# Kernel optimization log

Measured on AMD Instinct MI355X. Metric: run time of the kernel, lower is better.

The kernel has to match this reference:

```python
import jax, jax.numpy as jnp
import numpy as np

EPS = 1e-5

def _bn(x, g, b):
    # training-mode BatchNorm1d over the batch axis (axis 0), biased variance
    m = jnp.mean(x, axis=0)
    v = jnp.var(x, axis=0)
    return g * (x - m) / jnp.sqrt(v + EPS) + b

def _mlp(x, w1, b1, g1, be1, w2, b2, g2, be2, w3, b3):
    # Linear -> BN -> ReLU -> Linear -> BN -> ReLU -> Linear
    x = jax.nn.relu(_bn(x @ w1.T + b1, g1, be1))
    x = jax.nn.relu(_bn(x @ w2.T + b2, g2, be2))
    return x @ w3.T + b3

def setup_inputs() -> dict:
    key = jax.random.key(0)
    ks = jax.random.split(key, 10)
    B, S, D = 256, 512, 128
    w = lambda k: jax.random.normal(k, (D, D), jnp.float32) * 0.05
    return {
        "s": jax.random.normal(ks[0], (B, S, D), jnp.float32),
        "c": jax.random.normal(ks[1], (B, D), jnp.float32),
        "s_w1": w(ks[2]), "s_b1": jnp.zeros((D,), jnp.float32),
        "s_g1": jnp.ones((D,), jnp.float32), "s_be1": jnp.zeros((D,), jnp.float32),
        "s_w2": w(ks[3]), "s_b2": jnp.zeros((D,), jnp.float32),
        "s_g2": jnp.ones((D,), jnp.float32), "s_be2": jnp.zeros((D,), jnp.float32),
        "s_w3": w(ks[4]), "s_b3": jnp.zeros((D,), jnp.float32),
        "c_w1": w(ks[5]), "c_b1": jnp.zeros((D,), jnp.float32),
        "c_g1": jnp.ones((D,), jnp.float32), "c_be1": jnp.zeros((D,), jnp.float32),
        "c_w2": w(ks[6]), "c_b2": jnp.zeros((D,), jnp.float32),
        "c_g2": jnp.ones((D,), jnp.float32), "c_be2": jnp.zeros((D,), jnp.float32),
        "c_w3": w(ks[7]), "c_b3": jnp.zeros((D,), jnp.float32),
    }

def reference(s, c,
              s_w1, s_b1, s_g1, s_be1, s_w2, s_b2, s_g2, s_be2, s_w3, s_b3,
              c_w1, c_b1, c_g1, c_be1, c_w2, c_b2, c_g2, c_be2, c_w3, c_b3):
    # c_mlp: [B, D] -> [B, D] (BN over batch)
    c_out = _mlp(c, c_w1, c_b1, c_g1, c_be1, c_w2, c_b2, c_g2, c_be2, c_w3, c_b3)
    # s_mlp applied per sequence slice; BN stats over batch axis 0 only
    # (matches the torch loop where each s[:, i, :] gets its own BN stats).
    # s: [B, S, D]; _bn with axis=0 gives per-(slice, feature) stats.
    s_h = _mlp(s, s_w1, s_b1, s_g1, s_be1, s_w2, s_b2, s_g2, s_be2, s_w3, s_b3)
    s_out = s_h * c_out[:, None, :]          # context gate, [B, S, D]
    aggregated_c = jnp.max(s_out, axis=1)    # pooling == 'max', [B, D]
    return (s_out, aggregated_c)
```

## Files before the change

### kernel.cpp

```cpp
#include <hip/hip_runtime.h>
#include <hip/hip_bf16.h>

#define BATCH 256
#define SEQ   512
#define DIM   128
#define LDSK  136

typedef __attribute__((ext_vector_type(8))) __bf16  bf16x8;
typedef __attribute__((ext_vector_type(4))) __bf16  bf16x4;
typedef __attribute__((ext_vector_type(4))) float   f32x4;

template<int RT>
__device__ __forceinline__ void matmul_layer(
    const __bf16* __restrict__ Xa, const __bf16* __restrict__ wg,
    const float* __restrict__ bias, f32x4 (&acc)[RT][8], int wave, int m, int q)
{
  const int rowbase = wave * RT * 16;
#pragma unroll
  for (int ct = 0; ct < 8; ++ct) {
    const float b = bias[ct * 16 + m];
    const f32x4 bv = {b, b, b, b};
#pragma unroll
    for (int rt = 0; rt < RT; ++rt) acc[rt][ct] = bv;
  }
#pragma unroll
  for (int ks = 0; ks < 4; ++ks) {
    const int k0 = ks * 32 + q * 8;
    bf16x8 a[RT], bw[8];
#pragma unroll
    for (int rt = 0; rt < RT; ++rt)
      a[rt] = *(const bf16x8*)(Xa + (rowbase + rt * 16 + m) * LDSK + k0);
#pragma unroll
    for (int ct = 0; ct < 8; ++ct)
      bw[ct] = *(const bf16x8*)(wg + (ct * 16 + m) * DIM + k0);
#pragma unroll
    for (int rt = 0; rt < RT; ++rt)
#pragma unroll
      for (int ct = 0; ct < 8; ++ct)
        acc[rt][ct] = __builtin_amdgcn_mfma_f32_16x16x32_bf16(a[rt], bw[ct], acc[rt][ct], 0, 0, 0);
  }
}

template<int RT>
__device__ __forceinline__ void stats_accum(
    const f32x4 (&acc)[RT][8], float* sumA, float* sqA, int m, int q)
{
#pragma unroll
  for (int ct = 0; ct < 8; ++ct) {
    float s = 0.f, ss = 0.f;
#pragma unroll
    for (int rt = 0; rt < RT; ++rt)
#pragma unroll
      for (int r = 0; r < 4; ++r) { const float v = acc[rt][ct][r]; s += v; ss += v * v; }
    s  += __shfl_xor(s, 16, 64);  s  += __shfl_xor(s, 32, 64);
    ss += __shfl_xor(ss, 16, 64); ss += __shfl_xor(ss, 32, 64);
    if (q == 0) { atomicAdd(&sumA[ct * 16 + m], s); atomicAdd(&sqA[ct * 16 + m], ss); }
  }
}

__device__ __forceinline__ void bn_coefs(int tid, const float* __restrict__ g,
    const float* __restrict__ be, float* sumA, float* sqA, float* cA, float* cC)
{
  if (tid < DIM) {
    const float mean = sumA[tid] * (1.0f / BATCH);
    const float var  = sqA[tid]  * (1.0f / BATCH) - mean * mean;
    const float rstd = rsqrtf(var + 1e-5f);
    const float a = g[tid] * rstd;
    cA[tid] = a;
    cC[tid] = be[tid] - a * mean;
    sumA[tid] = 0.f; sqA[tid] = 0.f;
  }
}

template<int RT>
__device__ __forceinline__ void bn_relu_store(
    const f32x4 (&acc)[RT][8], __bf16* Xa, const float* cA, const float* cC,
    int wave, int m, int q)
{
  const int rowbase = wave * RT * 16;
#pragma unroll
  for (int ct = 0; ct < 8; ++ct) {
    const int n = ct * 16 + m;
    const float a = cA[n], c = cC[n];
#pragma unroll
    for (int rt = 0; rt < RT; ++rt)
#pragma unroll
      for (int r = 0; r < 4; ++r) {
        const float y = fmaxf(0.f, a * acc[rt][ct][r] + c);
        const int row = rowbase + rt * 16 + q * 4 + r;
        Xa[row * LDSK + n] = (__bf16)y;
      }
  }
}

template<int NW, bool GATE>
__global__ __launch_bounds__(NW * 64, 2)
void mlp_kernel(const float* __restrict__ xin, long xrow_stride,
                const __bf16* __restrict__ w1, const __bf16* __restrict__ w2,
                const __bf16* __restrict__ w3,
                const float* __restrict__ b1, const float* __restrict__ g1, const float* __restrict__ be1,
                const float* __restrict__ b2, const float* __restrict__ g2, const float* __restrict__ be2,
                const float* __restrict__ b3,
                const float* __restrict__ gate,
                float* __restrict__ out)
{
  const int tid  = threadIdx.x;
  constexpr int NT = NW * 64;
  constexpr int RT = 16 / NW;
  const int wave = tid >> 6, lane = tid & 63;
  const int m = lane & 15, q = lane >> 4;
  const int slice = GATE ? blockIdx.x : 0;
  const float* x0 = GATE ? (xin + (long)slice * DIM) : xin;

  __shared__ __bf16 Xa[BATCH * LDSK];
  __shared__ float sumA[DIM], sqA[DIM], cA[DIM], cC[DIM];

  for (int t = tid; t < DIM; t += NT) { sumA[t] = 0.f; sqA[t] = 0.f; }

  {
    const int rpi = NT / 32;
    const int r0  = tid >> 5;
    const int c4  = (tid & 31) * 4;
#pragma unroll
    for (int it = 0; it < BATCH / rpi; ++it) {
      const int r = it * rpi + r0;
      const float4 v = *(const float4*)(x0 + (long)r * xrow_stride + c4);
      bf16x4 h = { (__bf16)v.x, (__bf16)v.y, (__bf16)v.z, (__bf16)v.w };
      *(bf16x4*)(Xa + r * LDSK + c4) = h;
    }
  }
  __syncthreads();

  f32x4 acc[RT][8];

  matmul_layer<RT>(Xa, w1, b1, acc, wave, m, q);
  stats_accum<RT>(acc, sumA, sqA, m, q);
  __syncthreads();
  bn_coefs(tid, g1, be1, sumA, sqA, cA, cC);
  __syncthreads();
  bn_relu_store<RT>(acc, Xa, cA, cC, wave, m, q);
  __syncthreads();

  matmul_layer<RT>(Xa, w2, b2, acc, wave, m, q);
  stats_accum<RT>(acc, sumA, sqA, m, q);
  __syncthreads();
  bn_coefs(tid, g2, be2, sumA, sqA, cA, cC);
  __syncthreads();
  bn_relu_store<RT>(acc, Xa, cA, cC, wave, m, q);
  __syncthreads();

  matmul_layer<RT>(Xa, w3, b3, acc, wave, m, q);

  const int rowbase = wave * RT * 16;
#pragma unroll
  for (int ct = 0; ct < 8; ++ct) {
    const int col = ct * 16 + m;
#pragma unroll
    for (int rt = 0; rt < RT; ++rt) {
#pragma unroll
      for (int r = 0; r < 4; ++r) {
        const int row = rowbase + rt * 16 + q * 4 + r;
        float y = acc[rt][ct][r];
        if (GATE) {
          y *= gate[row * DIM + col];
          out[((long)row * SEQ + slice) * DIM + col] = y;
        } else {
          out[row * DIM + col] = y;
        }
      }
    }
  }
}

__global__ void prep_kernel(const float* __restrict__ w0, const float* __restrict__ w1,
                            const float* __restrict__ w2, const float* __restrict__ w3,
                            const float* __restrict__ w4, const float* __restrict__ w5,
                            __bf16* __restrict__ dst)
{
  const int idx = blockIdx.x * blockDim.x + threadIdx.x;
  const int mi  = idx >> 12;
  const int j   = (idx & 4095) * 4;
  const float* srcs[6] = {w0, w1, w2, w3, w4, w5};
  const float4 v = *(const float4*)(srcs[mi] + j);
  bf16x4 h = { (__bf16)v.x, (__bf16)v.y, (__bf16)v.z, (__bf16)v.w };
  *(bf16x4*)(dst + mi * 16384 + j) = h;
}

__global__ __launch_bounds__(512) void maxpool_kernel(
    const float* __restrict__ sout, float* __restrict__ agg)
{
  __shared__ float red[512];
  const int b = blockIdx.x;
  const int t = threadIdx.x;
  const int d = t & 127, ig = t >> 7;
  const float* p = sout + (long)b * SEQ * DIM + d;
  float m0 = -INFINITY, m1 = -INFINITY, m2 = -INFINITY, m3 = -INFINITY;
  const int i0 = ig * 128;
#pragma unroll 8
  for (int i = i0; i < i0 + 128; i += 4) {
    m0 = fmaxf(m0, p[(long)(i + 0) * DIM]);
    m1 = fmaxf(m1, p[(long)(i + 1) * DIM]);
    m2 = fmaxf(m2, p[(long)(i + 2) * DIM]);
    m3 = fmaxf(m3, p[(long)(i + 3) * DIM]);
  }
  red[t] = fmaxf(fmaxf(m0, m1), fmaxf(m2, m3));
  __syncthreads();
  if (t < 128) {
    const float a = fmaxf(fmaxf(red[t], red[t + 128]), fmaxf(red[t + 256], red[t + 384]));
    agg[b * DIM + t] = a;
  }
}

extern "C" void kernel_launch(void* const* d_in, const int* in_sizes, int n_in,
                              void* d_out, int out_size, void* d_ws, size_t ws_size,
                              hipStream_t stream)
{
  const float* s     = (const float*)d_in[0];
  const float* c     = (const float*)d_in[1];
  const float* s_w1  = (const float*)d_in[2];
  const float* s_b1  = (const float*)d_in[3];
  const float* s_g1  = (const float*)d_in[4];
  const float* s_be1 = (const float*)d_in[5];
  const float* s_w2  = (const float*)d_in[6];
  const float* s_b2  = (const float*)d_in[7];
  const float* s_g2  = (const float*)d_in[8];
  const float* s_be2 = (const float*)d_in[9];
  const float* s_w3  = (const float*)d_in[10];
  const float* s_b3  = (const float*)d_in[11];
  const float* c_w1  = (const float*)d_in[12];
  const float* c_b1  = (const float*)d_in[13];
  const float* c_g1  = (const float*)d_in[14];
  const float* c_be1 = (const float*)d_in[15];
  const float* c_w2  = (const float*)d_in[16];
  const float* c_b2  = (const float*)d_in[17];
  const float* c_g2  = (const float*)d_in[18];
  const float* c_be2 = (const float*)d_in[19];
  const float* c_w3  = (const float*)d_in[20];
  const float* c_b3  = (const float*)d_in[21];

  float* out   = (float*)d_out;
  float* c_out = (float*)d_ws;
  __bf16* wbf  = (__bf16*)((char*)d_ws + (size_t)BATCH * DIM * sizeof(float));

  prep_kernel<<<96, 256, 0, stream>>>(s_w1, s_w2, s_w3, c_w1, c_w2, c_w3, wbf);

  mlp_kernel<8, false><<<1, 512, 0, stream>>>(
      c, (long)DIM,
      wbf + 3 * 16384, wbf + 4 * 16384, wbf + 5 * 16384,
      c_b1, c_g1, c_be1, c_b2, c_g2, c_be2, c_b3,
      nullptr, c_out);

  mlp_kernel<4, true><<<SEQ, 256, 0, stream>>>(
      s, (long)SEQ * DIM,
      wbf, wbf + 16384, wbf + 2 * 16384,
      s_b1, s_g1, s_be1, s_b2, s_g2, s_be2, s_b3,
      c_out, out);

  maxpool_kernel<<<BATCH, 512, 0, stream>>>(out, out + (long)BATCH * SEQ * DIM);
}
```

Baseline: 225.4 us.

## Use 16 waves per slice, fuse weight conversion, drop barriers, vectorise maxpool

Each MLP block now uses 1024 threads with one 16-row tile per wave. Separate BN stat buffers let per-wave Xa row ownership remove several barriers, and BN coefficients are computed inline. The weight bf16 conversion moves into the c-MLP kernel, removing one launch, and the c-MLP reads float weights directly. Maxpool uses float4 loads. In exchange, each wave reloads the full weight fragments, which raises L2 traffic.

Result: slower. 376.4 us (+67.0%).

```diff
diff --git a/kernel.cpp b/kernel.cpp
--- a/kernel.cpp
+++ b/kernel.cpp
@@ -10,204 +10,181 @@
 typedef __attribute__((ext_vector_type(4))) __bf16  bf16x4;
 typedef __attribute__((ext_vector_type(4))) float   f32x4;
 
-template<int RT>
+__device__ __forceinline__ bf16x8 load_bfrag(const __bf16* __restrict__ wg, int n, int k0) {
+  return *(const bf16x8*)(wg + n * DIM + k0);
+}
+__device__ __forceinline__ bf16x8 load_bfrag(const float* __restrict__ wg, int n, int k0) {
+  const float4 v0 = *(const float4*)(wg + n * DIM + k0);
+  const float4 v1 = *(const float4*)(wg + n * DIM + k0 + 4);
+  bf16x8 r = { (__bf16)v0.x, (__bf16)v0.y, (__bf16)v0.z, (__bf16)v0.w,
+               (__bf16)v1.x, (__bf16)v1.y, (__bf16)v1.z, (__bf16)v1.w };
+  return r;
+}
+
+template<typename WT>
 __device__ __forceinline__ void matmul_layer(
-    const __bf16* __restrict__ Xa, const __bf16* __restrict__ wg,
-    const float* __restrict__ bias, f32x4 (&acc)[RT][8], int wave, int m, int q)
-{
-  const int rowbase = wave * RT * 16;
+    const __bf16* __restrict__ Xa, const WT* __restrict__ wg,
+    const float* __restrict__ bias, f32x4 (&acc)[8], int rowbase, int m, int q)
+{
 #pragma unroll
   for (int ct = 0; ct < 8; ++ct) {
     const float b = bias[ct * 16 + m];
-    const f32x4 bv = {b, b, b, b};
-#pragma unroll
-    for (int rt = 0; rt < RT; ++rt) acc[rt][ct] = bv;
+    acc[ct] = (f32x4){b, b, b, b};
   }
 #pragma unroll
   for (int ks = 0; ks < 4; ++ks) {
     const int k0 = ks * 32 + q * 8;
-    bf16x8 a[RT], bw[8];
-#pragma unroll
-    for (int rt = 0; rt < RT; ++rt)
-      a[rt] = *(const bf16x8*)(Xa + (rowbase + rt * 16 + m) * LDSK + k0);
-#pragma unroll
-    for (int ct = 0; ct < 8; ++ct)
-      bw[ct] = *(const bf16x8*)(wg + (ct * 16 + m) * DIM + k0);
-#pragma unroll
-    for (int rt = 0; rt < RT; ++rt)
-#pragma unroll
-      for (int ct = 0; ct < 8; ++ct)
-        acc[rt][ct] = __builtin_amdgcn_mfma_f32_16x16x32_bf16(a[rt], bw[ct], acc[rt][ct], 0, 0, 0);
-  }
-}
-
-template<int RT>
+    const bf16x8 a = *(const bf16x8*)(Xa + (rowbase + m) * LDSK + k0);
+#pragma unroll
+    for (int ct = 0; ct < 8; ++ct) {
+      const bf16x8 bw = load_bfrag(wg, ct * 16 + m, k0);
+      acc[ct] = __builtin_amdgcn_mfma_f32_16x16x32_bf16(a, bw, acc[ct], 0, 0, 0);
+    }
+  }
+}
+
 __device__ __forceinline__ void stats_accum(
-    const f32x4 (&acc)[RT][8], float* sumA, float* sqA, int m, int q)
+    const f32x4 (&acc)[8], float* sumA, float* sqA, int m, int q)
 {
 #pragma unroll
   for (int ct = 0; ct < 8; ++ct) {
     float s = 0.f, ss = 0.f;
 #pragma unroll
-    for (int rt = 0; rt < RT; ++rt)
-#pragma unroll
-      for (int r = 0; r < 4; ++r) { const float v = acc[rt][ct][r]; s += v; ss += v * v; }
+    for (int r = 0; r < 4; ++r) { const float v = acc[ct][r]; s += v; ss += v * v; }
     s  += __shfl_xor(s, 16, 64);  s  += __shfl_xor(s, 32, 64);
     ss += __shfl_xor(ss, 16, 64); ss += __shfl_xor(ss, 32, 64);
     if (q == 0) { atomicAdd(&sumA[ct * 16 + m], s); atomicAdd(&sqA[ct * 16 + m], ss); }
   }
 }
 
-__device__ __forceinline__ void bn_coefs(int tid, const float* __restrict__ g,
-    const float* __restrict__ be, float* sumA, float* sqA, float* cA, float* cC)
-{
-  if (tid < DIM) {
-    const float mean = sumA[tid] * (1.0f / BATCH);
-    const float var  = sqA[tid]  * (1.0f / BATCH) - mean * mean;
-    const float rstd = rsqrtf(var + 1e-5f);
-    const float a = g[tid] * rstd;
-    cA[tid] = a;
-    cC[tid] = be[tid] - a * mean;
-    sumA[tid] = 0.f; sqA[tid] = 0.f;
-  }
-}
-
-template<int RT>
 __device__ __forceinline__ void bn_relu_store(
-    const f32x4 (&acc)[RT][8], __bf16* Xa, const float* cA, const float* cC,
-    int wave, int m, int q)
-{
-  const int rowbase = wave * RT * 16;
+    const f32x4 (&acc)[8], __bf16* Xa, const float* sumA, const float* sqA,
+    const float* __restrict__ g, const float* __restrict__ be,
+    int rowbase, int m, int q)
+{
 #pragma unroll
   for (int ct = 0; ct < 8; ++ct) {
     const int n = ct * 16 + m;
-    const float a = cA[n], c = cC[n];
-#pragma unroll
-    for (int rt = 0; rt < RT; ++rt)
-#pragma unroll
-      for (int r = 0; r < 4; ++r) {
-        const float y = fmaxf(0.f, a * acc[rt][ct][r] + c);
-        const int row = rowbase + rt * 16 + q * 4 + r;
-        Xa[row * LDSK + n] = (__bf16)y;
-      }
-  }
-}
-
-template<int NW, bool GATE>
-__global__ __launch_bounds__(NW * 64, 2)
+    const float mean = sumA[n] * (1.0f / BATCH);
+    const float var  = sqA[n]  * (1.0f / BATCH) - mean * mean;
+    const float a = g[n] * rsqrtf(var + 1e-5f);
+    const float c = be[n] - a * mean;
+#pragma unroll
+    for (int r = 0; r < 4; ++r) {
+      const float y = fmaxf(0.f, a * acc[ct][r] + c);
+      Xa[(rowbase + q * 4 + r) * LDSK + n] = (__bf16)y;
+    }
+  }
+}
+
+template<typename WT, bool GATE, bool CONV>
+__global__ __launch_bounds__(1024, 4)
 void mlp_kernel(const float* __restrict__ xin, long xrow_stride,
-                const __bf16* __restrict__ w1, const __bf16* __restrict__ w2,
-                const __bf16* __restrict__ w3,
+                const WT* __restrict__ w1, const WT* __restrict__ w2, const WT* __restrict__ w3,
                 const float* __restrict__ b1, const float* __restrict__ g1, const float* __restrict__ be1,
                 const float* __restrict__ b2, const float* __restrict__ g2, const float* __restrict__ be2,
                 const float* __restrict__ b3,
+                const float* __restrict__ cw0, const float* __restrict__ cw1,
+                const float* __restrict__ cw2, __bf16* __restrict__ cvt_dst,
                 const float* __restrict__ gate,
                 float* __restrict__ out)
 {
   const int tid  = threadIdx.x;
-  constexpr int NT = NW * 64;
-  constexpr int RT = 16 / NW;
   const int wave = tid >> 6, lane = tid & 63;
   const int m = lane & 15, q = lane >> 4;
+  const int rowbase = wave * 16;
   const int slice = GATE ? blockIdx.x : 0;
   const float* x0 = GATE ? (xin + (long)slice * DIM) : xin;
 
   __shared__ __bf16 Xa[BATCH * LDSK];
-  __shared__ float sumA[DIM], sqA[DIM], cA[DIM], cC[DIM];
-
-  for (int t = tid; t < DIM; t += NT) { sumA[t] = 0.f; sqA[t] = 0.f; }
-
-  {
-    const int rpi = NT / 32;
-    const int r0  = tid >> 5;
-    const int c4  = (tid & 31) * 4;
-#pragma unroll
-    for (int it = 0; it < BATCH / rpi; ++it) {
-      const int r = it * rpi + r0;
-      const float4 v = *(const float4*)(x0 + (long)r * xrow_stride + c4);
+  __shared__ float sum0[DIM], sq0[DIM], sum1[DIM], sq1[DIM];
+
+  if (CONV) {
+    const float* srcs[3] = {cw0, cw1, cw2};
+#pragma unroll
+    for (int it = 0; it < 12; ++it) {
+      const int ci = it * 1024 + tid;
+      const int mi = ci >> 12;
+      const int j  = (ci & 4095) * 4;
+      const float4 v = *(const float4*)(srcs[mi] + j);
       bf16x4 h = { (__bf16)v.x, (__bf16)v.y, (__bf16)v.z, (__bf16)v.w };
-      *(bf16x4*)(Xa + r * LDSK + c4) = h;
-    }
-  }
-  __syncthreads();
-
-  f32x4 acc[RT][8];
-
-  matmul_layer<RT>(Xa, w1, b1, acc, wave, m, q);
-  stats_accum<RT>(acc, sumA, sqA, m, q);
-  __syncthreads();
-  bn_coefs(tid, g1, be1, sumA, sqA, cA, cC);
-  __syncthreads();
-  bn_relu_store<RT>(acc, Xa, cA, cC, wave, m, q);
-  __syncthreads();
-
-  matmul_layer<RT>(Xa, w2, b2, acc, wave, m, q);
-  stats_accum<RT>(acc, sumA, sqA, m, q);
-  __syncthreads();
-  bn_coefs(tid, g2, be2, sumA, sqA, cA, cC);
-  __syncthreads();
-  bn_relu_store<RT>(acc, Xa, cA, cC, wave, m, q);
-  __syncthreads();
-
-  matmul_layer<RT>(Xa, w3, b3, acc, wave, m, q);
-
-  const int rowbase = wave * RT * 16;
+      *(bf16x4*)(cvt_dst + mi * 16384 + j) = h;
+    }
+  }
+
+#pragma unroll
+  for (int it = 0; it < 4; ++it) {
+    const int row = rowbase + it * 4 + (lane >> 4);
+    const int col = (lane & 15) * 8;
+    const float* src = x0 + (long)row * xrow_stride + col;
+    const float4 v0 = *(const float4*)src;
+    const float4 v1 = *(const float4*)(src + 4);
+    bf16x8 h = { (__bf16)v0.x, (__bf16)v0.y, (__bf16)v0.z, (__bf16)v0.w,
+                 (__bf16)v1.x, (__bf16)v1.y, (__bf16)v1.z, (__bf16)v1.w };
+    *(bf16x8*)(Xa + row * LDSK + col) = h;
+  }
+  if (tid < DIM) { sum0[tid] = 0.f; sq0[tid] = 0.f; sum1[tid] = 0.f; sq1[tid] = 0.f; }
+  __syncthreads();
+
+  f32x4 acc[8];
+
+  matmul_layer(Xa, w1, b1, acc, rowbase, m, q);
+  stats_accum(acc, sum0, sq0, m, q);
+  __syncthreads();
+  bn_relu_store(acc, Xa, sum0, sq0, g1, be1, rowbase, m, q);
+
+  matmul_layer(Xa, w2, b2, acc, rowbase, m, q);
+  stats_accum(acc, sum1, sq1, m, q);
+  __syncthreads();
+  bn_relu_store(acc, Xa, sum1, sq1, g2, be2, rowbase, m, q);
+
+  matmul_layer(Xa, w3, b3, acc, rowbase, m, q);
+
 #pragma unroll
   for (int ct = 0; ct < 8; ++ct) {
     const int col = ct * 16 + m;
 #pragma unroll
-    for (int rt = 0; rt < RT; ++rt) {
-#pragma unroll
-      for (int r = 0; r < 4; ++r) {
-        const int row = rowbase + rt * 16 + q * 4 + r;
-        float y = acc[rt][ct][r];
-        if (GATE) {
-          y *= gate[row * DIM + col];
-          out[((long)row * SEQ + slice) * DIM + col] = y;
-        } else {
-          out[row * DIM + col] = y;
-        }
+    for (int r = 0; r < 4; ++r) {
+      const int row = rowbase + q * 4 + r;
+      float y = acc[ct][r];
+      if (GATE) {
+        y *= gate[row * DIM + col];
+        out[((long)row * SEQ + slice) * DIM + col] = y;
+      } else {
+        out[row * DIM + col] = y;
       }
     }
   }
 }
 
-__global__ void prep_kernel(const float* __restrict__ w0, const float* __restrict__ w1,
-                            const float* __restrict__ w2, const float* __restrict__ w3,
-                            const float* __restrict__ w4, const float* __restrict__ w5,
-                            __bf16* __restrict__ dst)
-{
-  const int idx = blockIdx.x * blockDim.x + threadIdx.x;
-  const int mi  = idx >> 12;
-  const int j   = (idx & 4095) * 4;
-  const float* srcs[6] = {w0, w1, w2, w3, w4, w5};
-  const float4 v = *(const float4*)(srcs[mi] + j);
-  bf16x4 h = { (__bf16)v.x, (__bf16)v.y, (__bf16)v.z, (__bf16)v.w };
-  *(bf16x4*)(dst + mi * 16384 + j) = h;
+__device__ __forceinline__ float4 vmax4(float4 a, float4 b) {
+  return (float4){fmaxf(a.x, b.x), fmaxf(a.y, b.y), fmaxf(a.z, b.z), fmaxf(a.w, b.w)};
 }
 
 __global__ __launch_bounds__(512) void maxpool_kernel(
     const float* __restrict__ sout, float* __restrict__ agg)
 {
-  __shared__ float red[512];
+  __shared__ float4 red[512];
   const int b = blockIdx.x;
   const int t = threadIdx.x;
-  const int d = t & 127, ig = t >> 7;
-  const float* p = sout + (long)b * SEQ * DIM + d;
-  float m0 = -INFINITY, m1 = -INFINITY, m2 = -INFINITY, m3 = -INFINITY;
-  const int i0 = ig * 128;
+  const int d4 = (t & 31) * 4;
+  const int ig = t >> 5;
+  const float* p = sout + (long)b * SEQ * DIM + d4;
+  float4 m0 = {-INFINITY, -INFINITY, -INFINITY, -INFINITY};
+  float4 m1 = m0;
+  const int i0 = ig * 32;
 #pragma unroll 8
-  for (int i = i0; i < i0 + 128; i += 4) {
-    m0 = fmaxf(m0, p[(long)(i + 0) * DIM]);
-    m1 = fmaxf(m1, p[(long)(i + 1) * DIM]);
-    m2 = fmaxf(m2, p[(long)(i + 2) * DIM]);
-    m3 = fmaxf(m3, p[(long)(i + 3) * DIM]);
-  }
-  red[t] = fmaxf(fmaxf(m0, m1), fmaxf(m2, m3));
-  __syncthreads();
-  if (t < 128) {
-    const float a = fmaxf(fmaxf(red[t], red[t + 128]), fmaxf(red[t + 256], red[t + 384]));
-    agg[b * DIM + t] = a;
+  for (int i = i0; i < i0 + 32; i += 2) {
+    m0 = vmax4(m0, *(const float4*)(p + (long)(i + 0) * DIM));
+    m1 = vmax4(m1, *(const float4*)(p + (long)(i + 1) * DIM));
+  }
+  red[t] = vmax4(m0, m1);
+  __syncthreads();
+  if (t < 32) {
+    float4 a = red[t];
+#pragma unroll
+    for (int g = 1; g < 16; ++g) a = vmax4(a, red[g * 32 + t]);
+    *(float4*)(agg + b * DIM + t * 4) = a;
   }
 }
 
@@ -242,18 +219,18 @@
   float* c_out = (float*)d_ws;
   __bf16* wbf  = (__bf16*)((char*)d_ws + (size_t)BATCH * DIM * sizeof(float));
 
-  prep_kernel<<<96, 256, 0, stream>>>(s_w1, s_w2, s_w3, c_w1, c_w2, c_w3, wbf);
-
-  mlp_kernel<8, false><<<1, 512, 0, stream>>>(
+  mlp_kernel<float, false, true><<<1, 1024, 0, stream>>>(
       c, (long)DIM,
-      wbf + 3 * 16384, wbf + 4 * 16384, wbf + 5 * 16384,
+      c_w1, c_w2, c_w3,
       c_b1, c_g1, c_be1, c_b2, c_g2, c_be2, c_b3,
+      s_w1, s_w2, s_w3, wbf,
       nullptr, c_out);
 
-  mlp_kernel<4, true><<<SEQ, 256, 0, stream>>>(
+  mlp_kernel<__bf16, true, false><<<SEQ, 1024, 0, stream>>>(
       s, (long)SEQ * DIM,
       wbf, wbf + 16384, wbf + 2 * 16384,
       s_b1, s_g1, s_be1, s_b2, s_g2, s_be2, s_b3,
+      nullptr, nullptr, nullptr, nullptr,
       c_out, out);
 
   maxpool_kernel<<<BATCH, 512, 0, stream>>>(out, out + (long)BATCH * SEQ * DIM);
```
